# Kernel optimization log

Hardware: AMD Instinct MI355X
Metric: run time of the kernel (lower is better)

Reference implementation:

```python
import jax, jax.numpy as jnp
import numpy as np
import math

DIM = 3      # coordinate dim per node
N_NODES = 15 # 45 / 3
HEADS = 3
D_K = 1


def _spatial_graph():
    # ST-GCN style 15-joint skeleton: (self, inward, outward) adjacency, shape (3,15,15)
    edges = [(1, 0), (2, 1), (3, 2), (4, 0), (5, 4), (6, 5), (7, 0),
             (8, 7), (9, 8), (10, 9), (11, 8), (12, 11), (13, 8), (14, 13)]
    self_a = np.eye(N_NODES, dtype=np.float32)
    inward = np.zeros((N_NODES, N_NODES), dtype=np.float32)
    for i, j in edges:
        inward[i, j] = 1.0
    outward = inward.T.copy()
    return jnp.asarray(np.stack([self_a, inward, outward], axis=0))


def setup_inputs() -> dict:
    key = jax.random.key(0)
    ks = jax.random.split(key, 11)
    bs, T, F = 32, 2048, DIM * N_NODES
    bound3 = 1.0 / math.sqrt(DIM)
    bound45 = 1.0 / math.sqrt(F)
    return {
        "q": jax.random.normal(ks[0], (bs, T, F), jnp.float32),
        "k": jax.random.normal(ks[1], (bs, T, F), jnp.float32),
        "v": jax.random.normal(ks[2], (bs, T, F), jnp.float32),
        "wq": jax.random.uniform(ks[3], (DIM, DIM), jnp.float32, -bound3, bound3),
        "bq": jax.random.uniform(ks[4], (DIM,), jnp.float32, -bound3, bound3),
        "wk": jax.random.uniform(ks[5], (DIM, DIM), jnp.float32, -bound3, bound3),
        "bk": jax.random.uniform(ks[6], (DIM,), jnp.float32, -bound3, bound3),
        "wv": jax.random.uniform(ks[7], (DIM, DIM), jnp.float32, -bound3, bound3),
        "bv": jax.random.uniform(ks[8], (DIM,), jnp.float32, -bound3, bound3),
        "wo": jax.random.uniform(ks[9], (F, F), jnp.float32, -bound45, bound45),
        "bo": jax.random.uniform(ks[10], (F,), jnp.float32, -bound45, bound45),
        "graph": _spatial_graph(),
        "is_test": 0,
    }


def _project(x, w, b, bs, T):
    # (bs,T,45) -> (bs,T,3,15) -> (bs,T,15,3) -> linear -> (bs,T,15,3,1) -> (bs,T,3,15,1)
    x = x.reshape(bs, T, DIM, N_NODES).transpose(0, 1, 3, 2)
    x = x @ w.T + b
    return x.reshape(bs, T, N_NODES, HEADS, D_K).transpose(0, 1, 3, 2, 4)


def reference(q, k, v, wq, bq, wk, bk, wv, bv, wo, bo, graph, is_test):
    bs, T, F = q.shape
    qh = _project(q, wq, bq, bs, T)  # (bs,T,h,15,1)
    kh = _project(k, wk, bk, bs, T)
    vh = _project(v, wv, bv, bs, T)
    # abs scores with graph mask, shape (bs,T,h,15,15)
    scores = jnp.abs(jnp.einsum('bthnd,bthmd->bthnm', qh, kh) / math.sqrt(D_K))
    graph_tot = graph.sum(0)  # (15,15)
    scores = jnp.where(graph_tot == 0, jnp.float32(-1e9), scores)
    # softmax over flattened 15*15 grid
    att = jax.nn.softmax(scores.reshape(bs, T, HEADS, N_NODES * N_NODES), axis=-1)
    att = att.reshape(bs, T, HEADS, N_NODES, N_NODES)
    out = jnp.einsum('bthnm,bthmd->bthnd', att, vh)  # (bs,T,h,15,1)
    concat = out.transpose(0, 1, 3, 2, 4).reshape(bs, T, F)
    return concat @ wo.T + bo
```

## Files before the change

### kernel.cpp

```cpp
#include <hip/hip_runtime.h>


#define SLAB 2880

__device__ __forceinline__ void glds16(const float* g, float* l) {
  __builtin_amdgcn_global_load_lds(
      (const __attribute__((address_space(1))) void*)g,
      (__attribute__((address_space(3))) void*)l, 16, 0, 0);
}

__global__ void __launch_bounds__(192)
mha_spatial_kernel(const float* __restrict__ q, const float* __restrict__ k,
                   const float* __restrict__ v,
                   const float* __restrict__ wq, const float* __restrict__ bq,
                   const float* __restrict__ wk, const float* __restrict__ bk,
                   const float* __restrict__ wv, const float* __restrict__ bv,
                   const float* __restrict__ wo, const float* __restrict__ bo,
                   float* __restrict__ out)
{
  constexpr int MOFF[16] = {0,4,7,10,12,15,18,20,23,28,31,33,36,38,41,43};
  constexpr int MN[43] = {0,1,4,7,  0,1,2,  1,2,3,  2,3,  0,4,5,  4,5,6,
                          5,6,  0,7,8,  7,8,9,11,13,  8,9,10,  9,10,
                          8,11,12,  11,12,  8,13,14,  13,14};

  __shared__ float sm[3 * SLAB];
  const int tid = threadIdx.x;
  const int p = tid & 63;
  const int h = __builtin_amdgcn_readfirstlane(tid >> 6);
  const size_t base = (size_t)blockIdx.x * SLAB;

  {
    const float* gq = q + base;
    const float* gk = k + base;
    float* l0 = sm;
    float* l1 = sm + SLAB;
#pragma unroll
    for (int i = 0; i < 4; ++i) {
      const int idx = i * 192 + tid;
      if (idx < 720) {
        const int off = idx * 4;
        glds16(gq + off, l0 + off);
        glds16(gk + off, l1 + off);
      }
    }
  }

  const float wq0 = wq[h*3+0], wq1 = wq[h*3+1], wq2 = wq[h*3+2], bq0 = bq[h];
  const float wk0 = wk[h*3+0], wk1 = wk[h*3+1], wk2 = wk[h*3+2], bk0 = bk[h];
  const float wv0 = wv[h*3+0], wv1 = wv[h*3+1], wv2 = wv[h*3+2], bv0 = bv[h];

  __syncthreads();

  {
    const float* gv = v + base;
    float* l2 = sm + 2 * SLAB;
#pragma unroll
    for (int i = 0; i < 4; ++i) {
      const int idx = i * 192 + tid;
      if (idx < 720) glds16(gv + idx * 4, l2 + idx * 4);
    }
  }

  float e[43];
  float rz;
  {
    const float* xq = sm + p * 45;
    const float* xk = sm + SLAB + p * 45;
    float aq[15];
#pragma unroll
    for (int n = 0; n < 15; ++n)
      aq[n] = fabsf(bq0 + xq[n] * wq0 + xq[15 + n] * wq1 + xq[30 + n] * wq2);
    float Z0 = 0.0f, Z1 = 0.0f;
#pragma unroll
    for (int m = 0; m < 15; ++m) {
      const float akm = fabsf(bk0 + xk[m] * wk0 + xk[15 + m] * wk1 + xk[30 + m] * wk2);
#pragma unroll
      for (int t = MOFF[m]; t < MOFF[m + 1]; ++t) {
        const float et = __expf(aq[MN[t]] * akm);
        e[t] = et;
        if (t & 1) Z1 += et; else Z0 += et;
      }
    }
    rz = 1.0f / (Z0 + Z1);
  }

  __syncthreads();

  float oh[15];
  {
    const float* xv = sm + 2 * SLAB + p * 45;
#pragma unroll
    for (int n = 0; n < 15; ++n) oh[n] = 0.0f;
#pragma unroll
    for (int m = 0; m < 15; ++m) {
      const float vvm = bv0 + xv[m] * wv0 + xv[15 + m] * wv1 + xv[30 + m] * wv2;
#pragma unroll
      for (int t = MOFF[m]; t < MOFF[m + 1]; ++t)
        oh[MN[t]] += e[t] * vvm;
    }
  }

  {
    float* crow = sm + p * 45;
#pragma unroll
    for (int n = 0; n < 15; ++n)
      crow[n * 3 + h] = oh[n] * rz;
  }
  __syncthreads();

  {
    const int fbase = h * 15;
    const float* crow = sm + p * 45;
    float acc[15];
#pragma unroll
    for (int j = 0; j < 15; ++j) acc[j] = bo[fbase + j];
#pragma unroll
    for (int c = 0; c < 3; ++c) {
      float cg[15];
#pragma unroll
      for (int t = 0; t < 15; ++t) cg[t] = crow[c * 15 + t];
#pragma unroll
      for (int t = 0; t < 15; ++t) {
#pragma unroll
        for (int j = 0; j < 15; ++j)
          acc[j] = fmaf(cg[t], wo[(fbase + j) * 45 + c * 15 + t], acc[j]);
      }
    }
    float* yrow = sm + SLAB + p * 45;
#pragma unroll
    for (int j = 0; j < 15; ++j) yrow[fbase + j] = acc[j];
  }
  __syncthreads();

  float* gout = out + base;
  const float* ysrc = sm + SLAB;
#pragma unroll
  for (int i = 0; i < 4; ++i) {
    const int idx = i * 192 + tid;
    if (idx < 720)
      *(float4*)(gout + idx * 4) = *(const float4*)(ysrc + idx * 4);
  }
}

extern "C" void kernel_launch(void* const* d_in, const int* in_sizes, int n_in,
                              void* d_out, int out_size, void* d_ws, size_t ws_size,
                              hipStream_t stream) {
  const float* q  = (const float*)d_in[0];
  const float* k  = (const float*)d_in[1];
  const float* v  = (const float*)d_in[2];
  const float* wq = (const float*)d_in[3];
  const float* bq = (const float*)d_in[4];
  const float* wk = (const float*)d_in[5];
  const float* bk = (const float*)d_in[6];
  const float* wv = (const float*)d_in[7];
  const float* bv = (const float*)d_in[8];
  const float* wo = (const float*)d_in[9];
  const float* bo = (const float*)d_in[10];
  float* out = (float*)d_out;

  hipLaunchKernelGGL(mha_spatial_kernel, dim3(1024), dim3(192), 0, stream,
                     q, k, v, wq, bq, wk, bk, wv, bv, wo, bo, out);
}
```

Before: 19.13 us.

## Interleave heads across adjacent lanes and pad concat rows for vector LDS reads

```diff
diff --git a/kernel.cpp b/kernel.cpp
--- a/kernel.cpp
+++ b/kernel.cpp
@@ -2,6 +2,8 @@
 
 
 #define SLAB 2880
+#define CROW 52
+#define YBASE 3328
 
 __device__ __forceinline__ void glds16(const float* g, float* l) {
   __builtin_amdgcn_global_load_lds(
@@ -25,9 +27,10 @@
 
   __shared__ float sm[3 * SLAB];
   const int tid = threadIdx.x;
-  const int p = tid & 63;
-  const int h = __builtin_amdgcn_readfirstlane(tid >> 6);
   const size_t base = (size_t)blockIdx.x * SLAB;
+
+  const int p3 = tid / 3;
+  const int h3 = tid - 3 * p3;
 
   {
     const float* gq = q + base;
@@ -45,9 +48,9 @@
     }
   }
 
-  const float wq0 = wq[h*3+0], wq1 = wq[h*3+1], wq2 = wq[h*3+2], bq0 = bq[h];
-  const float wk0 = wk[h*3+0], wk1 = wk[h*3+1], wk2 = wk[h*3+2], bk0 = bk[h];
-  const float wv0 = wv[h*3+0], wv1 = wv[h*3+1], wv2 = wv[h*3+2], bv0 = bv[h];
+  const float wq0 = wq[h3*3+0], wq1 = wq[h3*3+1], wq2 = wq[h3*3+2], bq0 = bq[h3];
+  const float wk0 = wk[h3*3+0], wk1 = wk[h3*3+1], wk2 = wk[h3*3+2], bk0 = bk[h3];
+  const float wv0 = wv[h3*3+0], wv1 = wv[h3*3+1], wv2 = wv[h3*3+2], bv0 = bv[h3];
 
   __syncthreads();
 
@@ -64,8 +67,8 @@
   float e[43];
   float rz;
   {
-    const float* xq = sm + p * 45;
-    const float* xk = sm + SLAB + p * 45;
+    const float* xq = sm + p3 * 45;
+    const float* xk = sm + SLAB + p3 * 45;
     float aq[15];
 #pragma unroll
     for (int n = 0; n < 15; ++n)
@@ -86,9 +89,9 @@
 
   __syncthreads();
 
-  float oh[15];
   {
-    const float* xv = sm + 2 * SLAB + p * 45;
+    const float* xv = sm + 2 * SLAB + p3 * 45;
+    float oh[15];
 #pragma unroll
     for (int n = 0; n < 15; ++n) oh[n] = 0.0f;
 #pragma unroll
@@ -98,42 +101,41 @@
       for (int t = MOFF[m]; t < MOFF[m + 1]; ++t)
         oh[MN[t]] += e[t] * vvm;
     }
-  }
-
-  {
-    float* crow = sm + p * 45;
+    float* crow = sm + p3 * CROW;
 #pragma unroll
     for (int n = 0; n < 15; ++n)
-      crow[n * 3 + h] = oh[n] * rz;
+      crow[n * 3 + h3] = oh[n] * rz;
   }
   __syncthreads();
 
   {
-    const int fbase = h * 15;
-    const float* crow = sm + p * 45;
+    const int p = tid & 63;
+    const int w = __builtin_amdgcn_readfirstlane(tid >> 6);
+    const int fbase = w * 15;
+    float cg[48];
+    const float4* c4 = (const float4*)(sm + p * CROW);
+#pragma unroll
+    for (int c = 0; c < 12; ++c) {
+      const float4 t = c4[c];
+      cg[c*4+0] = t.x; cg[c*4+1] = t.y; cg[c*4+2] = t.z; cg[c*4+3] = t.w;
+    }
     float acc[15];
 #pragma unroll
     for (int j = 0; j < 15; ++j) acc[j] = bo[fbase + j];
 #pragma unroll
-    for (int c = 0; c < 3; ++c) {
-      float cg[15];
+    for (int g = 0; g < 45; ++g) {
 #pragma unroll
-      for (int t = 0; t < 15; ++t) cg[t] = crow[c * 15 + t];
-#pragma unroll
-      for (int t = 0; t < 15; ++t) {
-#pragma unroll
-        for (int j = 0; j < 15; ++j)
-          acc[j] = fmaf(cg[t], wo[(fbase + j) * 45 + c * 15 + t], acc[j]);
-      }
+      for (int j = 0; j < 15; ++j)
+        acc[j] = fmaf(cg[g], wo[(fbase + j) * 45 + g], acc[j]);
     }
-    float* yrow = sm + SLAB + p * 45;
+    float* yrow = sm + YBASE + p * 45;
 #pragma unroll
     for (int j = 0; j < 15; ++j) yrow[fbase + j] = acc[j];
   }
   __syncthreads();
 
   float* gout = out + base;
-  const float* ysrc = sm + SLAB;
+  const float* ysrc = sm + YBASE;
 #pragma unroll
   for (int i = 0; i < 4; ++i) {
     const int idx = i * 192 + tid;
```

Result: faster. 18.46 us (-3.5%).
